# Performance work log

Hardware: AMD Instinct MI355X
Metric: run time of the kernel (lower is better)

Reference implementation:

```python
import jax, jax.numpy as jnp
import numpy as np

N, E, G = 50000, 600000, 512
F_IN, H, OUT = 128, 128, 256


def setup_inputs() -> dict:
    key = jax.random.key(0)
    ks = jax.random.split(key, 16)
    x = jax.random.normal(ks[0], (N, F_IN), dtype=jnp.float32)
    edge_index = jax.random.randint(ks[1], (2, E), 0, N, dtype=jnp.int64)
    batch = jnp.sort(jax.random.randint(ks[2], (N,), 0, G, dtype=jnp.int64))
    def lin(k, out_d, in_d):
        s = 1.0 / np.sqrt(in_d)
        return jax.random.uniform(k, (out_d, in_d), jnp.float32, -s, s)
    W1l, W1r = lin(ks[3], H, F_IN), lin(ks[4], H, F_IN)
    b1 = jnp.zeros((H,), jnp.float32)
    W2l, W2r = lin(ks[5], H, H), lin(ks[6], H, H)
    b2 = jnp.zeros((H,), jnp.float32)
    W3l, W3r = lin(ks[7], H, H), lin(ks[8], H, H)
    b3 = jnp.zeros((H,), jnp.float32)
    Wlin = lin(ks[9], OUT, 2 * H)
    blin = jnp.zeros((OUT,), jnp.float32)
    return dict(x=x, edge_index=edge_index, batch=batch,
                W1l=W1l, b1=b1, W1r=W1r, W2l=W2l, b2=b2, W2r=W2r,
                W3l=W3l, b3=b3, W3r=W3r, Wlin=Wlin, blin=blin)


def reference(x, edge_index, batch, W1l, b1, W1r, W2l, b2, W2r, W3l, b3, W3r, Wlin, blin):
    src, dst = edge_index[0], edge_index[1]
    # in-degree of each target node (mean aggregation denominator)
    deg = jax.ops.segment_sum(jnp.ones((E,), x.dtype), dst, num_segments=N)
    deg = jnp.maximum(deg, 1.0)[:, None]

    def sage(h, Wl, bl, Wr):
        # mean-aggregate neighbor features then linear; plus root transform
        agg = jax.ops.segment_sum(h[src], dst, num_segments=N) / deg
        return agg @ Wl.T + bl + h @ Wr.T

    h = jax.nn.relu(sage(x, W1l, b1, W1r))
    h = jax.nn.relu(sage(h, W2l, b2, W2r))
    h = sage(h, W3l, b3, W3r)

    # global max / mean pool per graph
    x_max = jax.ops.segment_max(h, batch, num_segments=G)
    x_max = jnp.where(jnp.isfinite(x_max), x_max, 0.0)
    cnt = jnp.maximum(jax.ops.segment_sum(jnp.ones((N,), h.dtype), batch, num_segments=G), 1.0)
    x_mean = jax.ops.segment_sum(h, batch, num_segments=G) / cnt[:, None]

    pooled = jnp.concatenate([x_max, x_mean], axis=1)  # [G, 2H]
    # dropout is identity in eval mode
    return pooled @ Wlin.T + blin
```

## Files before the change

kernel.cpp:

```cpp
#include <hip/hip_runtime.h>
#include <hip/hip_bf16.h>
#include <hip/hip_fp16.h>


#define FH 128
#define OUTD 256
#define SLOTS 64
#define PWB 96

typedef unsigned int u32;
typedef unsigned short u16;
typedef __attribute__((ext_vector_type(8))) _Float16 f16frag;
typedef __attribute__((ext_vector_type(4))) float f4frag;

typedef __attribute__((address_space(3))) u32 lds_u32;
typedef __attribute__((address_space(1))) const u32 glb_u32;

__device__ inline void async_copy16(const void* g, void* l) {
    __builtin_amdgcn_global_load_lds((glb_u32*)g, (lds_u32*)l, 16, 0, 0);
}

__global__ void mega_prep(const float* __restrict__ x, u16* __restrict__ x16, int n4,
                          const float* __restrict__ W0, const float* __restrict__ W1,
                          const float* __restrict__ W2, const float* __restrict__ W3,
                          const float* __restrict__ W4, const float* __restrict__ W5,
                          uint4* __restrict__ Bf,
                          const int* __restrict__ src, const int* __restrict__ dst,
                          int* __restrict__ cursor, int* __restrict__ esrc, int E, int SC,
                          const int* __restrict__ batch, int* __restrict__ gstart,
                          int n, int g, int GBND) {
    int blk = blockIdx.x;
    if (blk < PWB) {
        int wid = blk * 4 + (threadIdx.x >> 6);
        int pair = wid >> 3;
        int ot = wid & 7;
        int ks = pair & 7;
        int arr = pair >> 3;
        int l = threadIdx.x & 63;
        const float* Ws[6] = {W0, W1, W2, W3, W4, W5};
        const float* W = Ws[arr];
        bool use_lo = (ks >= 4);
        int kb = (ks & 3) * 32 + (l >> 4) * 8;
        int o = ot * 16 + (l & 15);
        float4 v0 = *(const float4*)(W + o * 128 + kb);
        float4 v1 = *(const float4*)(W + o * 128 + kb + 4);
        float vv[8] = {v0.x, v0.y, v0.z, v0.w, v1.x, v1.y, v1.z, v1.w};
        u32 h[8];
        #pragma unroll
        for (int i = 0; i < 8; ++i) {
            float v = vv[i];
            __half hi = __float2half(v);
            if (use_lo) {
                float rem = v - __half2float(hi);
                __half lo = __float2half(rem);
                h[i] = *(u16*)&lo;
            } else {
                h[i] = *(u16*)&hi;
            }
        }
        uint4 u;
        u.x = h[0] | (h[1] << 16);
        u.y = h[2] | (h[3] << 16);
        u.z = h[4] | (h[5] << 16);
        u.w = h[6] | (h[7] << 16);
        Bf[(size_t)arr * 4096 + (ks * 8 + ot) * 64 + l] = u;
    } else if (blk < PWB + SC) {
        int e = (blk - PWB) * 1024 + threadIdx.x * 4;
        if (e + 3 < E) {
            int4 dv = *(const int4*)(dst + e);
            int4 sv = *(const int4*)(src + e);
            int p0 = atomicAdd(&cursor[dv.x], 1);
            int p1 = atomicAdd(&cursor[dv.y], 1);
            int p2 = atomicAdd(&cursor[dv.z], 1);
            int p3 = atomicAdd(&cursor[dv.w], 1);
            if (p0 < SLOTS) esrc[(size_t)dv.x * SLOTS + p0] = sv.x;
            if (p1 < SLOTS) esrc[(size_t)dv.y * SLOTS + p1] = sv.y;
            if (p2 < SLOTS) esrc[(size_t)dv.z * SLOTS + p2] = sv.z;
            if (p3 < SLOTS) esrc[(size_t)dv.w * SLOTS + p3] = sv.w;
        } else {
            for (int k = 0; k < 4; ++k) {
                int ee = e + k;
                if (ee < E) {
                    int d = dst[ee];
                    int pos = atomicAdd(&cursor[d], 1);
                    if (pos < SLOTS) esrc[(size_t)d * SLOTS + pos] = src[ee];
                }
            }
        }
    } else if (blk < PWB + SC + GBND) {
        int i = (blk - PWB - SC) * 256 + threadIdx.x;
        if (i >= n) return;
        int b = batch[i];
        int pb = (i == 0) ? -1 : batch[i - 1];
        for (int q = pb + 1; q <= b; ++q) gstart[q] = i;
        if (i == n - 1) {
            for (int q = b + 1; q <= g; ++q) gstart[q] = n;
        }
    } else {
        int id = (blk - PWB - SC - GBND) * 256 + threadIdx.x;
        if (id >= n4) return;
        float4 v = *(const float4*)(x + (size_t)id * 4);
        __half h0 = __float2half(v.x), h1 = __float2half(v.y);
        __half h2 = __float2half(v.z), h3 = __float2half(v.w);
        ushort4 s;
        s.x = *(u16*)&h0; s.y = *(u16*)&h1; s.z = *(u16*)&h2; s.w = *(u16*)&h3;
        *(ushort4*)(x16 + (size_t)id * 4) = s;
    }
}

__device__ inline void add8(float* a, uint4 u) {
    float2 f0 = __half22float2(*(__half2*)&u.x);
    float2 f1 = __half22float2(*(__half2*)&u.y);
    float2 f2 = __half22float2(*(__half2*)&u.z);
    float2 f3 = __half22float2(*(__half2*)&u.w);
    a[0] += f0.x; a[1] += f0.y; a[2] += f1.x; a[3] += f1.y;
    a[4] += f2.x; a[5] += f2.y; a[6] += f3.x; a[7] += f3.y;
}

__global__ void agg_kernel(const u16* __restrict__ h16,
                           const int* __restrict__ deg, const int* __restrict__ esrc,
                           u16* __restrict__ agg16, int n_nodes) {
    int node = blockIdx.x * 16 + (threadIdx.x >> 4);
    if (node >= n_nodes) return;
    int lane = threadIdx.x & 15;
    int f = lane * 8;
    int d = deg[node];
    int s0 = node * SLOTS, s1 = s0 + min(d, SLOTS);
    float a0[8] = {0, 0, 0, 0, 0, 0, 0, 0};
    float a1[8] = {0, 0, 0, 0, 0, 0, 0, 0};
    float a2[8] = {0, 0, 0, 0, 0, 0, 0, 0};
    float a3[8] = {0, 0, 0, 0, 0, 0, 0, 0};
    int j = s0;
    for (; j + 8 <= s1; j += 8) {
        int4 e0 = *(const int4*)(esrc + j);
        int4 e1 = *(const int4*)(esrc + j + 4);
        uint4 u0 = *(const uint4*)(h16 + (size_t)e0.x * FH + f);
        uint4 u1 = *(const uint4*)(h16 + (size_t)e0.y * FH + f);
        uint4 u2 = *(const uint4*)(h16 + (size_t)e0.z * FH + f);
        uint4 u3 = *(const uint4*)(h16 + (size_t)e0.w * FH + f);
        uint4 u4 = *(const uint4*)(h16 + (size_t)e1.x * FH + f);
        uint4 u5 = *(const uint4*)(h16 + (size_t)e1.y * FH + f);
        uint4 u6 = *(const uint4*)(h16 + (size_t)e1.z * FH + f);
        uint4 u7 = *(const uint4*)(h16 + (size_t)e1.w * FH + f);
        add8(a0, u0); add8(a1, u1); add8(a2, u2); add8(a3, u3);
        add8(a0, u4); add8(a1, u5); add8(a2, u6); add8(a3, u7);
    }
    if (j + 4 <= s1) {
        int4 e0 = *(const int4*)(esrc + j);
        uint4 u0 = *(const uint4*)(h16 + (size_t)e0.x * FH + f);
        uint4 u1 = *(const uint4*)(h16 + (size_t)e0.y * FH + f);
        uint4 u2 = *(const uint4*)(h16 + (size_t)e0.z * FH + f);
        uint4 u3 = *(const uint4*)(h16 + (size_t)e0.w * FH + f);
        add8(a0, u0); add8(a1, u1); add8(a2, u2); add8(a3, u3);
        j += 4;
    }
    for (; j < s1; ++j) {
        uint4 u0 = *(const uint4*)(h16 + (size_t)esrc[j] * FH + f);
        add8(a0, u0);
    }
    float di = 1.0f / (float)max(d, 1);
    u32 oh[8];
    #pragma unroll
    for (int i = 0; i < 8; ++i) {
        __half hv = __float2half((a0[i] + a1[i] + a2[i] + a3[i]) * di);
        oh[i] = *(u16*)&hv;
    }
    uint4 w;
    w.x = oh[0] | (oh[1] << 16);
    w.y = oh[2] | (oh[3] << 16);
    w.z = oh[4] | (oh[5] << 16);
    w.w = oh[6] | (oh[7] << 16);
    *(uint4*)(agg16 + (size_t)node * FH + f) = w;
}

__global__ __launch_bounds__(256, 2)
void mfma_gemm(const u16* __restrict__ A1, const u16* __restrict__ A2,
               const uint4* __restrict__ Bf1, const uint4* __restrict__ Bf2,
               const float* __restrict__ bias, u16* __restrict__ out16,
               int do_relu) {
    __shared__ uint4 Bl[4096];
    int tid = threadIdx.x;
    int l = tid & 63;
    int wv = tid >> 6;
    int bn0 = blockIdx.x * 192 + wv * 48;
    int m = l & 15, q = l >> 4;

    f4frag acc[3][8];
    #pragma unroll
    for (int i = 0; i < 3; ++i)
        #pragma unroll
        for (int o = 0; o < 8; ++o)
            acc[i][o] = (f4frag){0.f, 0.f, 0.f, 0.f};

    #pragma unroll
    for (int p = 0; p < 2; ++p) {
        const u16* P = p ? A2 : A1;
        const uint4* Bf = p ? Bf2 : Bf1;

        f16frag Af[3][4];
        #pragma unroll
        for (int nt = 0; nt < 3; ++nt)
            #pragma unroll
            for (int s = 0; s < 4; ++s)
                Af[nt][s] = *(const f16frag*)(P + (size_t)(bn0 + nt * 16 + m) * FH + s * 32 + q * 8);

        __syncthreads();

        #pragma unroll
        for (int u = 0; u < 16; ++u)
            async_copy16(Bf + (size_t)u * 256 + wv * 64 + l,
                         &Bl[u * 256 + wv * 64]);
        __syncthreads();

        #pragma unroll
        for (int s = 0; s < 4; ++s) {
            {
                f16frag B[8];
                #pragma unroll
                for (int ot = 0; ot < 8; ++ot)
                    B[ot] = *(const f16frag*)&Bl[(size_t)(s * 8 + ot) * 64 + l];
                #pragma unroll
                for (int ot = 0; ot < 8; ++ot)
                    #pragma unroll
                    for (int nt = 0; nt < 3; ++nt)
                        acc[nt][ot] = __builtin_amdgcn_mfma_f32_16x16x32_f16(Af[nt][s], B[ot], acc[nt][ot], 0, 0, 0);
            }
            {
                f16frag B[8];
                #pragma unroll
                for (int ot = 0; ot < 8; ++ot)
                    B[ot] = *(const f16frag*)&Bl[(size_t)((s + 4) * 8 + ot) * 64 + l];
                #pragma unroll
                for (int ot = 0; ot < 8; ++ot)
                    #pragma unroll
                    for (int nt = 0; nt < 3; ++nt)
                        acc[nt][ot] = __builtin_amdgcn_mfma_f32_16x16x32_f16(Af[nt][s], B[ot], acc[nt][ot], 0, 0, 0);
            }
        }
    }

    #pragma unroll
    for (int nt = 0; nt < 3; ++nt)
        #pragma unroll
        for (int r = 0; r < 4; ++r) {
            int node = bn0 + nt * 16 + q * 4 + r;
            #pragma unroll
            for (int ot = 0; ot < 8; ++ot) {
                float v = acc[nt][ot][r] + bias[ot * 16 + m];
                if (do_relu) v = fmaxf(v, 0.f);
                __half hv = __float2half(v);
                out16[(size_t)node * FH + ot * 16 + m] = *(u16*)&hv;
            }
        }
}

__global__ __launch_bounds__(256, 2)
void pool_final(const u16* __restrict__ h16, const int* __restrict__ gstart,
                const float* __restrict__ Wlin, const float* __restrict__ blin,
                float* __restrict__ out) {
    __shared__ float smax[16][FH];
    __shared__ float ssum[16][FH];
    __shared__ float pr[2 * FH];
    int g = blockIdx.x;
    int tid = threadIdx.x;
    int way = tid >> 4;
    int lane = tid & 15;
    int f = lane * 8;
    int s = gstart[g], e = gstart[g + 1];

    float mx[8], sm[8];
    #pragma unroll
    for (int i = 0; i < 8; ++i) { mx[i] = -INFINITY; sm[i] = 0.f; }
    for (int n = s + way; n < e; n += 16) {
        uint4 u = *(const uint4*)(h16 + (size_t)n * FH + f);
        float2 f0 = __half22float2(*(__half2*)&u.x);
        float2 f1 = __half22float2(*(__half2*)&u.y);
        float2 f2 = __half22float2(*(__half2*)&u.z);
        float2 f3 = __half22float2(*(__half2*)&u.w);
        float v[8] = {f0.x, f0.y, f1.x, f1.y, f2.x, f2.y, f3.x, f3.y};
        #pragma unroll
        for (int i = 0; i < 8; ++i) {
            mx[i] = fmaxf(mx[i], v[i]);
            sm[i] += v[i];
        }
    }
    #pragma unroll
    for (int i = 0; i < 8; ++i) {
        smax[way][f + i] = mx[i];
        ssum[way][f + i] = sm[i];
    }
    __syncthreads();
    int c = e - s;
    if (tid < FH) {
        float m2 = -INFINITY, s2 = 0.f;
        #pragma unroll
        for (int w2 = 0; w2 < 16; ++w2) {
            m2 = fmaxf(m2, smax[w2][tid]);
            s2 += ssum[w2][tid];
        }
        pr[tid] = (c > 0) ? m2 : 0.f;
        pr[FH + tid] = s2 / (float)max(c, 1);
    }
    __syncthreads();
    int o = tid;
    const float4* wr = (const float4*)(Wlin + (size_t)o * (2 * FH));
    float acc = 0.f;
    #pragma unroll
    for (int j = 0; j < (2 * FH) / 4; ++j) {
        float4 wv = wr[j];
        acc += wv.x * pr[j * 4 + 0] + wv.y * pr[j * 4 + 1] +
               wv.z * pr[j * 4 + 2] + wv.w * pr[j * 4 + 3];
    }
    out[(size_t)g * OUTD + o] = acc + blin[o];
}

extern "C" void kernel_launch(void* const* d_in, const int* in_sizes, int n_in,
                              void* d_out, int out_size, void* d_ws, size_t ws_size,
                              hipStream_t stream) {
    const float* x     = (const float*)d_in[0];
    const int*   ei    = (const int*)d_in[1];
    const int*   batch = (const int*)d_in[2];
    const float* W1l = (const float*)d_in[3];
    const float* b1  = (const float*)d_in[4];
    const float* W1r = (const float*)d_in[5];
    const float* W2l = (const float*)d_in[6];
    const float* b2  = (const float*)d_in[7];
    const float* W2r = (const float*)d_in[8];
    const float* W3l = (const float*)d_in[9];
    const float* b3  = (const float*)d_in[10];
    const float* W3r = (const float*)d_in[11];
    const float* Wlin = (const float*)d_in[12];
    const float* blin = (const float*)d_in[13];
    float* out = (float*)d_out;

    const int E = in_sizes[1] / 2;
    const int N = in_sizes[2];
    const int G = out_size / OUTD;
    const int* src = ei;
    const int* dst = ei + E;
    const int GB = (N + 191) / 192;
    const int NP = GB * 192;

    char* w = (char*)d_ws;
    auto alloc = [&](size_t bytes) {
        void* p = (void*)w;
        w += (bytes + 255) & ~(size_t)255;
        return p;
    };
    int*   cursor = (int*)alloc((size_t)N * sizeof(int));
    int*   esrc   = (int*)alloc((size_t)N * SLOTS * sizeof(int));
    int*   gstart = (int*)alloc((size_t)(G + 1) * sizeof(int));
    u16*   x16    = (u16*)alloc((size_t)NP * FH * sizeof(u16));
    u16*   agg16  = (u16*)alloc((size_t)NP * FH * sizeof(u16));
    u16*   hA16   = (u16*)alloc((size_t)NP * FH * sizeof(u16));
    u16*   hB16   = (u16*)alloc((size_t)NP * FH * sizeof(u16));
    uint4* BF     = (uint4*)alloc((size_t)6 * 4096 * sizeof(uint4));
    (void)ws_size;

    hipMemsetAsync(cursor, 0, (size_t)N * sizeof(int), stream);
    const int n4 = N * 32;
    const int PX = (n4 + 255) / 256;
    const int SC = (E + 1023) / 1024;
    const int GBND = (N + 255) / 256;
    mega_prep<<<PWB + SC + GBND + PX, 256, 0, stream>>>(
        x, x16, n4,
        W1l, W1r, W2l, W2r, W3l, W3r, BF,
        src, dst, cursor, esrc, E, SC,
        batch, gstart, N, G, GBND);

    const int agg_grid = (N + 15) / 16;

    agg_kernel<<<agg_grid, 256, 0, stream>>>(x16, cursor, esrc, agg16, N);
    mfma_gemm<<<GB, 256, 0, stream>>>(agg16, x16, BF + 0 * 4096, BF + 1 * 4096, b1, hA16, 1);
    agg_kernel<<<agg_grid, 256, 0, stream>>>(hA16, cursor, esrc, agg16, N);
    mfma_gemm<<<GB, 256, 0, stream>>>(agg16, hA16, BF + 2 * 4096, BF + 3 * 4096, b2, hB16, 1);
    agg_kernel<<<agg_grid, 256, 0, stream>>>(hB16, cursor, esrc, agg16, N);
    mfma_gemm<<<GB, 256, 0, stream>>>(agg16, hB16, BF + 4 * 4096, BF + 5 * 4096, b3, hA16, 0);

    pool_final<<<G, 256, 0, stream>>>(hA16, gstart, Wlin, blin, out);
}
```

Baseline: 285.0 us.

## Bucket each node's neighbor list by source-index range for gather locality

```diff
diff --git a/kernel.cpp b/kernel.cpp
--- a/kernel.cpp
+++ b/kernel.cpp
@@ -5,13 +5,15 @@
 
 #define FH 128
 #define OUTD 256
-#define SLOTS 64
+#define NR 7
+#define SR 16
 #define PWB 96
 
 typedef unsigned int u32;
 typedef unsigned short u16;
 typedef __attribute__((ext_vector_type(8))) _Float16 f16frag;
 typedef __attribute__((ext_vector_type(4))) float f4frag;
+typedef __attribute__((ext_vector_type(4))) u32 u32x4;
 
 typedef __attribute__((address_space(3))) u32 lds_u32;
 typedef __attribute__((address_space(1))) const u32 glb_u32;
@@ -69,21 +71,27 @@
         if (e + 3 < E) {
             int4 dv = *(const int4*)(dst + e);
             int4 sv = *(const int4*)(src + e);
-            int p0 = atomicAdd(&cursor[dv.x], 1);
-            int p1 = atomicAdd(&cursor[dv.y], 1);
-            int p2 = atomicAdd(&cursor[dv.z], 1);
-            int p3 = atomicAdd(&cursor[dv.w], 1);
-            if (p0 < SLOTS) esrc[(size_t)dv.x * SLOTS + p0] = sv.x;
-            if (p1 < SLOTS) esrc[(size_t)dv.y * SLOTS + p1] = sv.y;
-            if (p2 < SLOTS) esrc[(size_t)dv.z * SLOTS + p2] = sv.z;
-            if (p3 < SLOTS) esrc[(size_t)dv.w * SLOTS + p3] = sv.w;
+            int f0 = dv.x * NR + min(sv.x >> 13, NR - 1);
+            int f1 = dv.y * NR + min(sv.y >> 13, NR - 1);
+            int f2 = dv.z * NR + min(sv.z >> 13, NR - 1);
+            int f3 = dv.w * NR + min(sv.w >> 13, NR - 1);
+            int p0 = atomicAdd(&cursor[f0], 1);
+            int p1 = atomicAdd(&cursor[f1], 1);
+            int p2 = atomicAdd(&cursor[f2], 1);
+            int p3 = atomicAdd(&cursor[f3], 1);
+            if (p0 < SR) esrc[(size_t)f0 * SR + p0] = sv.x;
+            if (p1 < SR) esrc[(size_t)f1 * SR + p1] = sv.y;
+            if (p2 < SR) esrc[(size_t)f2 * SR + p2] = sv.z;
+            if (p3 < SR) esrc[(size_t)f3 * SR + p3] = sv.w;
         } else {
             for (int k = 0; k < 4; ++k) {
                 int ee = e + k;
                 if (ee < E) {
                     int d = dst[ee];
-                    int pos = atomicAdd(&cursor[d], 1);
-                    if (pos < SLOTS) esrc[(size_t)d * SLOTS + pos] = src[ee];
+                    int s = src[ee];
+                    int fb = d * NR + min(s >> 13, NR - 1);
+                    int pos = atomicAdd(&cursor[fb], 1);
+                    if (pos < SR) esrc[(size_t)fb * SR + pos] = s;
                 }
             }
         }
@@ -118,59 +126,49 @@
 }
 
 __global__ void agg_kernel(const u16* __restrict__ h16,
-                           const int* __restrict__ deg, const int* __restrict__ esrc,
+                           const int* __restrict__ cnt, const int* __restrict__ esrc,
                            u16* __restrict__ agg16, int n_nodes) {
     int node = blockIdx.x * 16 + (threadIdx.x >> 4);
     if (node >= n_nodes) return;
     int lane = threadIdx.x & 15;
     int f = lane * 8;
-    int d = deg[node];
-    int s0 = node * SLOTS, s1 = s0 + min(d, SLOTS);
     float a0[8] = {0, 0, 0, 0, 0, 0, 0, 0};
     float a1[8] = {0, 0, 0, 0, 0, 0, 0, 0};
     float a2[8] = {0, 0, 0, 0, 0, 0, 0, 0};
-    float a3[8] = {0, 0, 0, 0, 0, 0, 0, 0};
-    int j = s0;
-    for (; j + 8 <= s1; j += 8) {
-        int4 e0 = *(const int4*)(esrc + j);
-        int4 e1 = *(const int4*)(esrc + j + 4);
-        uint4 u0 = *(const uint4*)(h16 + (size_t)e0.x * FH + f);
-        uint4 u1 = *(const uint4*)(h16 + (size_t)e0.y * FH + f);
-        uint4 u2 = *(const uint4*)(h16 + (size_t)e0.z * FH + f);
-        uint4 u3 = *(const uint4*)(h16 + (size_t)e0.w * FH + f);
-        uint4 u4 = *(const uint4*)(h16 + (size_t)e1.x * FH + f);
-        uint4 u5 = *(const uint4*)(h16 + (size_t)e1.y * FH + f);
-        uint4 u6 = *(const uint4*)(h16 + (size_t)e1.z * FH + f);
-        uint4 u7 = *(const uint4*)(h16 + (size_t)e1.w * FH + f);
-        add8(a0, u0); add8(a1, u1); add8(a2, u2); add8(a3, u3);
-        add8(a0, u4); add8(a1, u5); add8(a2, u6); add8(a3, u7);
-    }
-    if (j + 4 <= s1) {
-        int4 e0 = *(const int4*)(esrc + j);
-        uint4 u0 = *(const uint4*)(h16 + (size_t)e0.x * FH + f);
-        uint4 u1 = *(const uint4*)(h16 + (size_t)e0.y * FH + f);
-        uint4 u2 = *(const uint4*)(h16 + (size_t)e0.z * FH + f);
-        uint4 u3 = *(const uint4*)(h16 + (size_t)e0.w * FH + f);
-        add8(a0, u0); add8(a1, u1); add8(a2, u2); add8(a3, u3);
-        j += 4;
-    }
-    for (; j < s1; ++j) {
-        uint4 u0 = *(const uint4*)(h16 + (size_t)esrc[j] * FH + f);
-        add8(a0, u0);
+    int d = 0;
+    #pragma unroll
+    for (int r = 0; r < NR; ++r) {
+        int c = __builtin_nontemporal_load(cnt + (size_t)node * NR + r);
+        d += c;
+        int cc = min(c, SR);
+        const int* ep = esrc + ((size_t)node * NR + r) * SR;
+        int j = 0;
+        for (; j + 2 <= cc; j += 2) {
+            int i0 = __builtin_nontemporal_load(ep + j);
+            int i1 = __builtin_nontemporal_load(ep + j + 1);
+            uint4 u0 = *(const uint4*)(h16 + (size_t)i0 * FH + f);
+            uint4 u1 = *(const uint4*)(h16 + (size_t)i1 * FH + f);
+            add8(a0, u0); add8(a1, u1);
+        }
+        if (j < cc) {
+            int i0 = __builtin_nontemporal_load(ep + j);
+            uint4 u0 = *(const uint4*)(h16 + (size_t)i0 * FH + f);
+            add8(a2, u0);
+        }
     }
     float di = 1.0f / (float)max(d, 1);
     u32 oh[8];
     #pragma unroll
     for (int i = 0; i < 8; ++i) {
-        __half hv = __float2half((a0[i] + a1[i] + a2[i] + a3[i]) * di);
+        __half hv = __float2half((a0[i] + a1[i] + a2[i]) * di);
         oh[i] = *(u16*)&hv;
     }
-    uint4 w;
+    u32x4 w;
     w.x = oh[0] | (oh[1] << 16);
     w.y = oh[2] | (oh[3] << 16);
     w.z = oh[4] | (oh[5] << 16);
     w.w = oh[6] | (oh[7] << 16);
-    *(uint4*)(agg16 + (size_t)node * FH + f) = w;
+    __builtin_nontemporal_store(w, (u32x4*)(agg16 + (size_t)node * FH + f));
 }
 
 __global__ __launch_bounds__(256, 2)
@@ -347,8 +345,8 @@
         w += (bytes + 255) & ~(size_t)255;
         return p;
     };
-    int*   cursor = (int*)alloc((size_t)N * sizeof(int));
-    int*   esrc   = (int*)alloc((size_t)N * SLOTS * sizeof(int));
+    int*   cursor = (int*)alloc((size_t)N * NR * sizeof(int));
+    int*   esrc   = (int*)alloc((size_t)N * NR * SR * sizeof(int));
     int*   gstart = (int*)alloc((size_t)(G + 1) * sizeof(int));
     u16*   x16    = (u16*)alloc((size_t)NP * FH * sizeof(u16));
     u16*   agg16  = (u16*)alloc((size_t)NP * FH * sizeof(u16));
@@ -357,7 +355,7 @@
     uint4* BF     = (uint4*)alloc((size_t)6 * 4096 * sizeof(uint4));
     (void)ws_size;
 
-    hipMemsetAsync(cursor, 0, (size_t)N * sizeof(int), stream);
+    (void)hipMemsetAsync(cursor, 0, (size_t)N * NR * sizeof(int), stream);
     const int n4 = N * 32;
     const int PX = (n4 + 255) / 256;
     const int SC = (E + 1023) / 1024;
```

After: 349.2 us. 22.5% more time.
